# Kernel tuning notes

Measured on AMD Instinct MI355X. Metric: run time of the kernel, lower is better.

The kernel has to match this reference:

```python
import jax, jax.numpy as jnp
import numpy as np

MIN_NORM = 1e-15
EPS = 4e-3  # fp32 boundary epsilon used by HGCN PoincareBall


def _norm(x):
    return jnp.maximum(jnp.linalg.norm(x, axis=-1, keepdims=True), MIN_NORM)


def _artanh(x):
    return jnp.arctanh(jnp.clip(x, -1.0 + 1e-7, 1.0 - 1e-7))


def proj(x, c):
    # clip points to the open Poincare ball of curvature c
    norm = _norm(x)
    maxnorm = (1.0 - EPS) / jnp.sqrt(c)
    return jnp.where(norm > maxnorm, x / norm * maxnorm, x)


def expmap0(u, c):
    sc = jnp.sqrt(c)
    un = _norm(u)
    return jnp.tanh(sc * un) * u / (sc * un)


def logmap0(p, c):
    sc = jnp.sqrt(c)
    pn = _norm(p)
    return _artanh(sc * pn) * p / (pn * sc)


def mobius_add(x, y, c):
    x2 = jnp.sum(x * x, axis=-1, keepdims=True)
    y2 = jnp.sum(y * y, axis=-1, keepdims=True)
    xy = jnp.sum(x * y, axis=-1, keepdims=True)
    num = (1.0 + 2.0 * c * xy + c * y2) * x + (1.0 - c * x2) * y
    den = 1.0 + 2.0 * c * xy + (c ** 2) * x2 * y2
    return num / jnp.maximum(den, MIN_NORM)


def _mobius_from_mx(mx, x, c):
    # shared tail of mobius_matvec: mx is the Euclidean product, x the input points
    sc = jnp.sqrt(c)
    x_norm = _norm(x)            # [..., 1]
    mx_norm = _norm(mx)          # [..., 1]
    res = jnp.tanh(mx_norm / x_norm * _artanh(sc * x_norm)) * mx / (mx_norm * sc)
    zero_row = jnp.all(mx == 0, axis=-1, keepdims=True)
    return jnp.where(zero_row, jnp.zeros_like(res), res)


def mobius_matvec(m, x, c):
    # standard form: mx = x @ m^T   (m: [out, in], x: [N, in])
    return _mobius_from_mx(x @ m.T, x, c)


def hyp_linear(x, W, b, c):
    hw = proj(expmap0(W, c), c)             # proj_tan0 is identity on PoincareBall
    res = proj(mobius_matvec(hw, x, c), c)
    hb = proj(expmap0(b[None, :], c), c)
    return proj(mobius_add(res, hb, c), c)


def hyp_agg(h, adj, W, b, c):
    hw = proj(expmap0(W, c), c)
    support = mobius_matvec(hw, h, c)       # [N, O]
    # mobius_matvec(support, adj, c): Euclidean part is adj @ support,
    # hyperbolic rescale uses row norms of adj (the 'x' argument)
    out = _mobius_from_mx(adj @ support, adj, c)
    out = mobius_add(out, b[None, :], c)    # raw Euclidean bias, as in source
    return proj(out, c)


def hyp_act(h, c):
    xt = jax.nn.leaky_relu(logmap0(h, c))   # default slope 0.01 == F.leaky_relu
    return proj(expmap0(xt, c), 1.0 - c)    # NOTE: source projects with 1-c


def setup_inputs() -> dict:
    key = jax.random.key(0)
    kx, ka, kw1, kw2, kb2 = jax.random.split(key, 5)
    N, IN, OUT = 8192, 512, 128
    x = jax.random.normal(kx, (N, IN), dtype=jnp.float32) * 0.1
    adj = jax.random.uniform(ka, (N, N), dtype=jnp.float32) * (1.0 / N)
    c = jnp.full((1,), 0.7, dtype=jnp.float32)
    glorot = np.sqrt(6.0 / (IN + OUT))
    lin_weight = jax.random.uniform(kw1, (OUT, IN), minval=-glorot, maxval=glorot, dtype=jnp.float32)
    lin_bias = jnp.zeros((OUT,), dtype=jnp.float32)
    stdv = 1.0 / np.sqrt(OUT)
    agg_weight = jax.random.uniform(kw2, (OUT, OUT), minval=-stdv, maxval=stdv, dtype=jnp.float32)
    agg_bias = jax.random.uniform(kb2, (OUT,), minval=-stdv, maxval=stdv, dtype=jnp.float32)
    return {"x": x, "adj": adj, "c": c, "lin_weight": lin_weight, "lin_bias": lin_bias,
            "agg_weight": agg_weight, "agg_bias": agg_bias}


def reference(x, adj, c, lin_weight, lin_bias, agg_weight, agg_bias):
    h = hyp_linear(x, lin_weight, lin_bias, c)
    h = hyp_agg(h, adj, agg_weight, agg_bias, c)
    return hyp_act(h, c)
```

## Files before the change

### kernel.cpp

```cpp
#include <hip/hip_runtime.h>
#include <math.h>


#define MINN 1e-15f

typedef __bf16 bf16x8 __attribute__((ext_vector_type(8)));
typedef float  f32x4  __attribute__((ext_vector_type(4)));

__device__ __forceinline__ unsigned short f2bf(float f) {
  unsigned int u = __float_as_uint(f);
  u += 0x7FFFu + ((u >> 16) & 1u);
  return (unsigned short)(u >> 16);
}

__device__ __forceinline__ unsigned pk_trunc(float lo, float hi) {
  return __builtin_amdgcn_perm(__float_as_uint(hi), __float_as_uint(lo),
                               0x07060302u);
}

__device__ __forceinline__ float artanh_clip(float z) {
  const float B = (float)(1.0 - 1e-7);
  z = fminf(fmaxf(z, -B), B);
  return 0.5f * logf((1.0f + z) / (1.0f - z));
}

__device__ __forceinline__ float red16(float v) {
  v += __shfl_xor(v, 1, 16);
  v += __shfl_xor(v, 2, 16);
  v += __shfl_xor(v, 4, 16);
  v += __shfl_xor(v, 8, 16);
  return v;
}
__device__ __forceinline__ int red16_and(int v) {
  v &= __shfl_xor(v, 1, 16);
  v &= __shfl_xor(v, 2, 16);
  v &= __shfl_xor(v, 4, 16);
  v &= __shfl_xor(v, 8, 16);
  return v;
}
__device__ __forceinline__ float red8(float v) {
  v += __shfl_xor(v, 1, 8);
  v += __shfl_xor(v, 2, 8);
  v += __shfl_xor(v, 4, 8);
  return v;
}
__device__ __forceinline__ int red8_and(int v) {
  v &= __shfl_xor(v, 1, 8);
  v &= __shfl_xor(v, 2, 8);
  v &= __shfl_xor(v, 4, 8);
  return v;
}

__device__ __forceinline__ float block_reduce_128(float v, float* red, int t) {
  #pragma unroll
  for (int m = 1; m < 64; m <<= 1) v += __shfl_xor(v, m, 64);
  if ((t & 63) == 0) red[t >> 6] = v;
  __syncthreads();
  return red[0] + red[1];
}

__device__ __forceinline__ size_t bswz(int k, int n) {
  return ((size_t)(((k >> 5) * 8 + (n >> 4)) * 64 + ((k >> 3) & 3) * 16 +
                   (n & 15))) * 8 + (k & 7);
}

__global__ __launch_bounds__(128) void prep_kernel(
    const float* __restrict__ lw, const float* __restrict__ aw,
    const float* __restrict__ lb, const float* __restrict__ cp,
    unsigned short* __restrict__ B1, unsigned short* __restrict__ B2,
    float* __restrict__ hb)
{
  const float c  = cp[0];
  const float sc = sqrtf(c);
  const float maxn = 0.996f / sc;
  const int b = blockIdx.x, t = threadIdx.x;
  __shared__ float red[2];

  if (b < 128) {
    const int o = b;
    float4 v = ((const float4*)(lw + (size_t)o * 512))[t];
    float ss = block_reduce_128(v.x*v.x + v.y*v.y + v.z*v.z + v.w*v.w, red, t);
    float un = fmaxf(sqrtf(ss), MINN);
    float f  = tanhf(sc * un) / (sc * un);
    float nn = f * un;
    if (nn > maxn) f *= maxn / nn;
    float vals[4] = {v.x, v.y, v.z, v.w};
    #pragma unroll
    for (int i = 0; i < 4; ++i)
      B1[bswz(4 * t + i, o)] = f2bf(f * vals[i]);
  } else if (b < 256) {
    const int n = b - 128;
    float v = aw[(size_t)n * 128 + t];
    float ss = block_reduce_128(v * v, red, t);
    float un = fmaxf(sqrtf(ss), MINN);
    float f  = tanhf(sc * un) / (sc * un);
    float nn = f * un;
    if (nn > maxn) f *= maxn / nn;
    B2[bswz(t, n)] = f2bf(f * v);
  } else {
    float v = lb[t];
    float ss = block_reduce_128(v * v, red, t);
    float un = fmaxf(sqrtf(ss), MINN);
    float f  = tanhf(sc * un) / (sc * un);
    float nn = f * un;
    if (nn > maxn) f *= maxn / nn;
    hb[t] = f * v;
  }
}

__global__ __launch_bounds__(256, 2) void hyp_fused12(
    const float* __restrict__ x, const bf16x8* __restrict__ B1f,
    const bf16x8* __restrict__ B2f, const float* __restrict__ cp,
    const float* __restrict__ hbv, unsigned short* __restrict__ B3)
{
  __shared__ __align__(16) float part[4][16][132];
  __shared__ float asw[4][16];
  __shared__ __align__(16) unsigned short h_lds[16][136];
  const int t = threadIdx.x;
  const int w = t >> 6, lane = t & 63;
  const int quad = lane >> 4, l15 = lane & 15;
  const int row0 = blockIdx.x * 16;
  const float c = cp[0], sc = sqrtf(c), maxn = 0.996f / sc;

  f32x4 acc[8] = {};
  float as4[4] = {};
  const float*  Ap = x + (size_t)(row0 + l15) * 512 + w * 128 + quad * 8;
  const bf16x8* Bp = B1f + (size_t)(w * 4) * 512 + lane;

  #pragma unroll
  for (int s = 0; s < 4; ++s) {
    float4 x0 = *(const float4*)(Ap + s * 32);
    float4 x1 = *(const float4*)(Ap + s * 32 + 4);
    as4[0] = fmaf(x0.x, x0.x, fmaf(x0.y, x0.y, as4[0]));
    as4[1] = fmaf(x0.z, x0.z, fmaf(x0.w, x0.w, as4[1]));
    as4[2] = fmaf(x1.x, x1.x, fmaf(x1.y, x1.y, as4[2]));
    as4[3] = fmaf(x1.z, x1.z, fmaf(x1.w, x1.w, as4[3]));
    union { unsigned short us[8]; bf16x8 v; } pk;
    pk.us[0] = f2bf(x0.x); pk.us[1] = f2bf(x0.y);
    pk.us[2] = f2bf(x0.z); pk.us[3] = f2bf(x0.w);
    pk.us[4] = f2bf(x1.x); pk.us[5] = f2bf(x1.y);
    pk.us[6] = f2bf(x1.z); pk.us[7] = f2bf(x1.w);
    #pragma unroll
    for (int i = 0; i < 8; ++i)
      acc[i] = __builtin_amdgcn_mfma_f32_16x16x32_bf16(
                   pk.v, Bp[(size_t)s * 512 + i * 64], acc[i], 0, 0, 0);
  }
  float asum = (as4[0] + as4[1]) + (as4[2] + as4[3]);
  asum += __shfl_xor(asum, 16, 64);
  asum += __shfl_xor(asum, 32, 64);
  #pragma unroll
  for (int i = 0; i < 8; ++i)
    #pragma unroll
    for (int r = 0; r < 4; ++r)
      part[w][quad * 4 + r][i * 16 + l15] = acc[i][r];
  if (lane < 16) asw[w][l15] = asum;
  __syncthreads();

  const int row = t >> 4, j0 = t & 15;
  float v[8];
  #pragma unroll
  for (int i = 0; i < 8; ++i)
    v[i] = part[0][row][j0 * 8 + i] + part[1][row][j0 * 8 + i]
         + part[2][row][j0 * 8 + i] + part[3][row][j0 * 8 + i];
  const float xss = asw[0][row] + asw[1][row] + asw[2][row] + asw[3][row];

  float mxss_l = 0.f; int zf = 1;
  #pragma unroll
  for (int i = 0; i < 8; ++i) { mxss_l += v[i] * v[i]; zf &= (v[i] == 0.f); }
  const float mxss = red16(mxss_l);
  zf = red16_and(zf);

  const float xn  = fmaxf(sqrtf(xss), MINN);
  const float mxn = fmaxf(sqrtf(mxss), MINN);
  float f1 = 0.f;
  if (!zf) f1 = tanhf(mxn / xn * artanh_clip(sc * xn)) / (mxn * sc);

  float g = f1;
  {
    float rn = f1 * mxn;
    if (rn > maxn) g = f1 * (maxn / rn);
  }
  float yv[8];
  {
    float4 q0 = ((const float4*)hbv)[j0 * 2];
    float4 q1 = ((const float4*)hbv)[j0 * 2 + 1];
    yv[0]=q0.x; yv[1]=q0.y; yv[2]=q0.z; yv[3]=q0.w;
    yv[4]=q1.x; yv[5]=q1.y; yv[6]=q1.z; yv[7]=q1.w;
  }
  float xy_l = 0.f, y2_l = 0.f, o8[8];
  #pragma unroll
  for (int i = 0; i < 8; ++i) {
    o8[i] = g * v[i];
    xy_l += o8[i] * yv[i];
    y2_l += yv[i] * yv[i];
  }
  const float xy = red16(xy_l), y2 = red16(y2_l);
  const float x2 = g * g * mxss;
  const float den = fmaxf(1.0f + 2.0f * c * xy + c * c * x2 * y2, MINN);
  const float ca = (1.0f + 2.0f * c * xy + c * y2) / den;
  const float cb = (1.0f - c * x2) / den;
  float h8[8]; float hss_l = 0.f;
  #pragma unroll
  for (int i = 0; i < 8; ++i) {
    h8[i] = ca * o8[i] + cb * yv[i];
    hss_l += h8[i] * h8[i];
  }
  const float hss = red16(hss_l);
  const float hn  = fmaxf(sqrtf(hss), MINN);
  const float s2  = (hn > maxn) ? maxn / hn : 1.0f;
  const float hn2 = fmaxf(s2 * hn, MINN);

  {
    union { unsigned short us[8]; uint4 q; } hp;
    #pragma unroll
    for (int i = 0; i < 8; ++i) hp.us[i] = f2bf(s2 * h8[i]);
    *(uint4*)&h_lds[row][j0 * 8] = hp.q;
  }
  __syncthreads();

  const bf16x8 av2 = *(const bf16x8*)&h_lds[l15][w * 32 + quad * 8];
  f32x4 acc2[8] = {};
  #pragma unroll
  for (int i = 0; i < 8; ++i)
    acc2[i] = __builtin_amdgcn_mfma_f32_16x16x32_bf16(
                  av2, B2f[(size_t)(w * 8 + i) * 64 + lane], acc2[i], 0, 0, 0);
  #pragma unroll
  for (int i = 0; i < 8; ++i)
    #pragma unroll
    for (int r = 0; r < 4; ++r)
      part[w][quad * 4 + r][i * 16 + l15] = acc2[i][r];
  __syncthreads();

  float v2[8];
  #pragma unroll
  for (int i = 0; i < 8; ++i)
    v2[i] = part[0][row][j0 * 8 + i] + part[1][row][j0 * 8 + i]
          + part[2][row][j0 * 8 + i] + part[3][row][j0 * 8 + i];
  float m2l = 0.f; int zf2 = 1;
  #pragma unroll
  for (int i = 0; i < 8; ++i) { m2l += v2[i] * v2[i]; zf2 &= (v2[i] == 0.f); }
  const float mx2ss = red16(m2l);
  zf2 = red16_and(zf2);
  const float mx2n = fmaxf(sqrtf(mx2ss), MINN);
  float f2 = 0.f;
  if (!zf2) f2 = tanhf(mx2n / hn2 * artanh_clip(sc * hn2)) / (mx2n * sc);

  const int k = row0 + row;
  const size_t base = ((size_t)(((k >> 5) * 8 + (j0 >> 1)) * 64 +
                       ((k >> 3) & 3) * 16 + 8 * (j0 & 1))) * 8 + (k & 7);
  #pragma unroll
  for (int i = 0; i < 8; ++i)
    B3[base + (size_t)i * 8] = f2bf(f2 * v2[i]);
}

#define G3_COMPUTE(U)                                                        \
  {                                                                          \
    float4 x0 = a0[U], x1 = a1[U];                                           \
    as4[0] = fmaf(x0.x, x0.x, fmaf(x0.y, x0.y, as4[0]));                     \
    as4[1] = fmaf(x0.z, x0.z, fmaf(x0.w, x0.w, as4[1]));                     \
    as4[2] = fmaf(x1.x, x1.x, fmaf(x1.y, x1.y, as4[2]));                     \
    as4[3] = fmaf(x1.z, x1.z, fmaf(x1.w, x1.w, as4[3]));                     \
    union { unsigned u32[4]; bf16x8 v; } pk;                                 \
    pk.u32[0] = pk_trunc(x0.x, x0.y);                                        \
    pk.u32[1] = pk_trunc(x0.z, x0.w);                                        \
    pk.u32[2] = pk_trunc(x1.x, x1.y);                                        \
    pk.u32[3] = pk_trunc(x1.z, x1.w);                                        \
    _Pragma("unroll")                                                        \
    for (int i = 0; i < 8; ++i)                                              \
      acc[i] = __builtin_amdgcn_mfma_f32_16x16x32_bf16(pk.v, b[(U) & 3][i],  \
                                                       acc[i], 0, 0, 0);     \
  }

__global__ __launch_bounds__(256, 1) void hyp_gemm3(
    const float* __restrict__ A, const bf16x8* __restrict__ Bf,
    const float* __restrict__ cp, const float* __restrict__ yvec,
    float* __restrict__ out)
{
  __shared__ __align__(16) float part[4][16][132];
  __shared__ float asw[4][16];
  const int t = threadIdx.x;
  const int w = t >> 6, lane = t & 63;
  const int quad = lane >> 4, l15 = lane & 15;
  const int rh = w >> 1, kh = w & 1;
  const int rowbase = blockIdx.x * 32;
  const int row0 = rowbase + rh * 16;
  const float c = cp[0], sc = sqrtf(c), maxn = 0.996f / sc;

  const int k0w = kh * 4096;
  f32x4 acc[8] = {};
  float as4[4] = {};
  const float*  Ap = A + (size_t)(row0 + l15) * 8192 + k0w + quad * 8;
  const bf16x8* Bp = Bf + (size_t)(k0w >> 5) * 512 + lane;

  float4 a0[8], a1[8];
  bf16x8 b[4][8];
  #pragma unroll
  for (int p = 0; p < 8; ++p) {
    a0[p] = *(const float4*)(Ap + p * 32);
    a1[p] = *(const float4*)(Ap + p * 32 + 4);
  }
  #pragma unroll
  for (int p = 0; p < 4; ++p)
    #pragma unroll
    for (int i = 0; i < 8; ++i) b[p][i] = Bp[(size_t)p * 512 + i * 64];

  for (int s = 0; s < 120; s += 8) {
    #pragma unroll
    for (int u = 0; u < 8; ++u) {
      const int sv = s + u;
      G3_COMPUTE(u);
      a0[u] = *(const float4*)(Ap + (size_t)(sv + 8) * 32);
      a1[u] = *(const float4*)(Ap + (size_t)(sv + 8) * 32 + 4);
      #pragma unroll
      for (int i = 0; i < 8; ++i)
        b[u & 3][i] = Bp[(size_t)(sv + 4) * 512 + i * 64];
    }
  }
  #pragma unroll
  for (int u = 0; u < 8; ++u) {
    G3_COMPUTE(u);
    if (u < 4) {
      #pragma unroll
      for (int i = 0; i < 8; ++i)
        b[u & 3][i] = Bp[(size_t)(124 + u) * 512 + i * 64];
    }
  }

  float asum = (as4[0] + as4[1]) + (as4[2] + as4[3]);
  asum += __shfl_xor(asum, 16, 64);
  asum += __shfl_xor(asum, 32, 64);
  #pragma unroll
  for (int i = 0; i < 8; ++i)
    #pragma unroll
    for (int r = 0; r < 4; ++r)
      part[w][quad * 4 + r][i * 16 + l15] = acc[i][r];
  if (lane < 16) asw[w][l15] = asum;
  __syncthreads();

  const int row = t >> 3, j0 = t & 7;
  const int rh2 = row >> 4, rr = row & 15;
  float v[16];
  #pragma unroll
  for (int i = 0; i < 4; ++i) {
    float4 qa = *(const float4*)&part[rh2 * 2][rr][j0 * 16 + 4 * i];
    float4 qb = *(const float4*)&part[rh2 * 2 + 1][rr][j0 * 16 + 4 * i];
    v[4*i+0] = qa.x + qb.x; v[4*i+1] = qa.y + qb.y;
    v[4*i+2] = qa.z + qb.z; v[4*i+3] = qa.w + qb.w;
  }
  const float xss = asw[rh2 * 2][rr] + asw[rh2 * 2 + 1][rr];

  float mxss_l = 0.f; int zf = 1;
  #pragma unroll
  for (int i = 0; i < 16; ++i) { mxss_l += v[i] * v[i]; zf &= (v[i] == 0.f); }
  const float mxss = red8(mxss_l);
  zf = red8_and(zf);

  const float xn  = fmaxf(sqrtf(xss), MINN);
  const float mxn = fmaxf(sqrtf(mxss), MINN);
  float f1 = 0.f;
  if (!zf) f1 = tanhf(mxn / xn * artanh_clip(sc * xn)) / (mxn * sc);

  float yv[16];
  #pragma unroll
  for (int i = 0; i < 4; ++i) {
    float4 q = ((const float4*)yvec)[j0 * 4 + i];
    yv[4*i+0] = q.x; yv[4*i+1] = q.y; yv[4*i+2] = q.z; yv[4*i+3] = q.w;
  }

  float xy_l = 0.f, y2_l = 0.f, o16[16];
  #pragma unroll
  for (int i = 0; i < 16; ++i) {
    o16[i] = f1 * v[i];
    xy_l += o16[i] * yv[i];
    y2_l += yv[i] * yv[i];
  }
  const float xy = red8(xy_l), y2 = red8(y2_l);
  const float x2 = f1 * f1 * mxss;
  const float den = fmaxf(1.0f + 2.0f * c * xy + c * c * x2 * y2, MINN);
  const float ca = (1.0f + 2.0f * c * xy + c * y2) / den;
  const float cb = (1.0f - c * x2) / den;
  float h16[16]; float hss_l = 0.f;
  #pragma unroll
  for (int i = 0; i < 16; ++i) {
    h16[i] = ca * o16[i] + cb * yv[i];
    hss_l += h16[i] * h16[i];
  }
  const float hss = red8(hss_l);
  const float hn  = fmaxf(sqrtf(hss), MINN);
  const float s2  = (hn > maxn) ? maxn / hn : 1.0f;

  const float pn = fmaxf(s2 * hn, MINN);
  const float lf = artanh_clip(sc * pn) / (pn * sc);
  float xt[16]; float uss_l = 0.f;
  #pragma unroll
  for (int i = 0; i < 16; ++i) {
    float l = lf * (s2 * h16[i]);
    xt[i] = (l >= 0.f) ? l : 0.01f * l;
    uss_l += xt[i] * xt[i];
  }
  const float uss = red8(uss_l);
  const float un  = fmaxf(sqrtf(uss), MINN);
  const float ef  = tanhf(sc * un) / (sc * un);
  const float on  = ef * un;
  const float maxn2 = 0.996f / sqrtf(1.0f - c);
  const float s3 = (on > maxn2) ? maxn2 / on : 1.0f;

  float* orow = out + (size_t)(rowbase + row) * 128 + j0 * 16;
  #pragma unroll
  for (int i = 0; i < 4; ++i)
    *(float4*)(orow + 4 * i) = make_float4(
        s3 * ef * xt[4*i+0], s3 * ef * xt[4*i+1],
        s3 * ef * xt[4*i+2], s3 * ef * xt[4*i+3]);
}

extern "C" void kernel_launch(void* const* d_in, const int* in_sizes, int n_in,
                              void* d_out, int out_size, void* d_ws, size_t ws_size,
                              hipStream_t stream)
{
  const float* x   = (const float*)d_in[0];
  const float* adj = (const float*)d_in[1];
  const float* cp  = (const float*)d_in[2];
  const float* lw  = (const float*)d_in[3];
  const float* lb  = (const float*)d_in[4];
  const float* aw  = (const float*)d_in[5];
  const float* ab  = (const float*)d_in[6];
  float* out = (float*)d_out;

  char* ws = (char*)d_ws;
  unsigned short* B1sw = (unsigned short*)(ws);
  unsigned short* B2sw = (unsigned short*)(ws + 131072);
  unsigned short* B3sw = (unsigned short*)(ws + 163840);
  float*          hb   = (float*)(ws + 2260992);

  prep_kernel<<<257, 128, 0, stream>>>(lw, aw, lb, cp, B1sw, B2sw, hb);
  hyp_fused12<<<512, 256, 0, stream>>>(x, (const bf16x8*)B1sw,
                                       (const bf16x8*)B2sw, cp, hb, B3sw);
  hyp_gemm3<<<256, 256, 0, stream>>>(adj, (const bf16x8*)B3sw, cp, ab, out);
}
```

Before: 436.2 us.

## Restructure adjacency GEMM to stage A through double-buffered LDS with 8 waves

The big adj@support kernel moves from 4 waves holding fp32 A tiles and B fragments in registers, with a split-K reduction, to 8 waves. These waves cooperatively load A rows, convert them to bf16 and stage them in a double-buffered LDS tile. Each wave then computes a 16x32 output slice over the full K range, so the split-K partial sums are no longer needed. The goal is to cut register pressure, raise occupancy with launch_bounds(512,2), and give coalesced full-row A streaming. The cost is a barrier per K window, with B fragments now reloaded per wave instead of held in registers.

```diff
diff --git a/kernel.cpp b/kernel.cpp
--- a/kernel.cpp
+++ b/kernel.cpp
@@ -36,18 +36,6 @@
   v &= __shfl_xor(v, 2, 16);
   v &= __shfl_xor(v, 4, 16);
   v &= __shfl_xor(v, 8, 16);
-  return v;
-}
-__device__ __forceinline__ float red8(float v) {
-  v += __shfl_xor(v, 1, 8);
-  v += __shfl_xor(v, 2, 8);
-  v += __shfl_xor(v, 4, 8);
-  return v;
-}
-__device__ __forceinline__ int red8_and(int v) {
-  v &= __shfl_xor(v, 1, 8);
-  v &= __shfl_xor(v, 2, 8);
-  v &= __shfl_xor(v, 4, 8);
   return v;
 }
 
@@ -253,164 +241,162 @@
     B3[base + (size_t)i * 8] = f2bf(f2 * v2[i]);
 }
 
-#define G3_COMPUTE(U)                                                        \
-  {                                                                          \
-    float4 x0 = a0[U], x1 = a1[U];                                           \
-    as4[0] = fmaf(x0.x, x0.x, fmaf(x0.y, x0.y, as4[0]));                     \
-    as4[1] = fmaf(x0.z, x0.z, fmaf(x0.w, x0.w, as4[1]));                     \
-    as4[2] = fmaf(x1.x, x1.x, fmaf(x1.y, x1.y, as4[2]));                     \
-    as4[3] = fmaf(x1.z, x1.z, fmaf(x1.w, x1.w, as4[3]));                     \
-    union { unsigned u32[4]; bf16x8 v; } pk;                                 \
-    pk.u32[0] = pk_trunc(x0.x, x0.y);                                        \
-    pk.u32[1] = pk_trunc(x0.z, x0.w);                                        \
-    pk.u32[2] = pk_trunc(x1.x, x1.y);                                        \
-    pk.u32[3] = pk_trunc(x1.z, x1.w);                                        \
-    _Pragma("unroll")                                                        \
-    for (int i = 0; i < 8; ++i)                                              \
-      acc[i] = __builtin_amdgcn_mfma_f32_16x16x32_bf16(pk.v, b[(U) & 3][i],  \
-                                                       acc[i], 0, 0, 0);     \
-  }
-
-__global__ __launch_bounds__(256, 1) void hyp_gemm3(
+__global__ __launch_bounds__(512, 2) void hyp_gemm3(
     const float* __restrict__ A, const bf16x8* __restrict__ Bf,
     const float* __restrict__ cp, const float* __restrict__ yvec,
     float* __restrict__ out)
 {
-  __shared__ __align__(16) float part[4][16][132];
-  __shared__ float asw[4][16];
+  __shared__ __align__(16) unsigned short a_lds[2][32][264];
   const int t = threadIdx.x;
   const int w = t >> 6, lane = t & 63;
   const int quad = lane >> 4, l15 = lane & 15;
-  const int rh = w >> 1, kh = w & 1;
-  const int rowbase = blockIdx.x * 32;
-  const int row0 = rowbase + rh * 16;
+  const int wm = w >> 2, wn = w & 3;
+  const int row0 = blockIdx.x * 32;
   const float c = cp[0], sc = sqrtf(c), maxn = 0.996f / sc;
 
-  const int k0w = kh * 4096;
-  f32x4 acc[8] = {};
+  f32x4 acc[2] = {};
   float as4[4] = {};
-  const float*  Ap = A + (size_t)(row0 + l15) * 8192 + k0w + quad * 8;
-  const bf16x8* Bp = Bf + (size_t)(k0w >> 5) * 512 + lane;
-
-  float4 a0[8], a1[8];
-  bf16x8 b[4][8];
-  #pragma unroll
-  for (int p = 0; p < 8; ++p) {
-    a0[p] = *(const float4*)(Ap + p * 32);
-    a1[p] = *(const float4*)(Ap + p * 32 + 4);
-  }
-  #pragma unroll
-  for (int p = 0; p < 4; ++p)
-    #pragma unroll
-    for (int i = 0; i < 8; ++i) b[p][i] = Bp[(size_t)p * 512 + i * 64];
-
-  for (int s = 0; s < 120; s += 8) {
-    #pragma unroll
-    for (int u = 0; u < 8; ++u) {
-      const int sv = s + u;
-      G3_COMPUTE(u);
-      a0[u] = *(const float4*)(Ap + (size_t)(sv + 8) * 32);
-      a1[u] = *(const float4*)(Ap + (size_t)(sv + 8) * 32 + 4);
+  const float* Ap = A + (size_t)(row0 + 4 * w) * 8192 + lane * 4;
+  const bf16x8* Bw = Bf + (size_t)(2 * wn) * 64 + lane;
+
+  {
+    float4 aR[4];
+    #pragma unroll
+    for (int j = 0; j < 4; ++j) aR[j] = *(const float4*)(Ap + j * 8192);
+    #pragma unroll
+    for (int j = 0; j < 4; ++j) {
+      as4[j] = fmaf(aR[j].x, aR[j].x, fmaf(aR[j].y, aR[j].y,
+               fmaf(aR[j].z, aR[j].z, fmaf(aR[j].w, aR[j].w, as4[j]))));
+      *(uint2*)&a_lds[0][4 * w + j][lane * 4] =
+          make_uint2(pk_trunc(aR[j].x, aR[j].y), pk_trunc(aR[j].z, aR[j].w));
+    }
+  }
+  __syncthreads();
+
+  for (int win = 0; win < 32; ++win) {
+    const int cur = win & 1;
+    bf16x8 b[8][2];
+    #pragma unroll
+    for (int ks = 0; ks < 8; ++ks) {
+      b[ks][0] = Bw[(size_t)((win * 8 + ks) * 8 + 0) * 64];
+      b[ks][1] = Bw[(size_t)((win * 8 + ks) * 8 + 1) * 64];
+    }
+    float4 aR[4];
+    if (win < 31) {
       #pragma unroll
-      for (int i = 0; i < 8; ++i)
-        b[u & 3][i] = Bp[(size_t)(sv + 4) * 512 + i * 64];
+      for (int j = 0; j < 4; ++j)
+        aR[j] = *(const float4*)(Ap + j * 8192 + (size_t)(win + 1) * 256);
     }
-  }
-  #pragma unroll
-  for (int u = 0; u < 8; ++u) {
-    G3_COMPUTE(u);
-    if (u < 4) {
+    #pragma unroll
+    for (int ks = 0; ks < 8; ++ks) {
+      bf16x8 af = *(const bf16x8*)
+          &a_lds[cur][16 * wm + l15][ks * 32 + quad * 8];
+      acc[0] = __builtin_amdgcn_mfma_f32_16x16x32_bf16(af, b[ks][0], acc[0],
+                                                       0, 0, 0);
+      acc[1] = __builtin_amdgcn_mfma_f32_16x16x32_bf16(af, b[ks][1], acc[1],
+                                                       0, 0, 0);
+    }
+    if (win < 31) {
       #pragma unroll
-      for (int i = 0; i < 8; ++i)
-        b[u & 3][i] = Bp[(size_t)(124 + u) * 512 + i * 64];
+      for (int j = 0; j < 4; ++j) {
+        as4[j] = fmaf(aR[j].x, aR[j].x, fmaf(aR[j].y, aR[j].y,
+                 fmaf(aR[j].z, aR[j].z, fmaf(aR[j].w, aR[j].w, as4[j]))));
+        *(uint2*)&a_lds[cur ^ 1][4 * w + j][lane * 4] =
+            make_uint2(pk_trunc(aR[j].x, aR[j].y), pk_trunc(aR[j].z, aR[j].w));
+      }
     }
-  }
-
-  float asum = (as4[0] + as4[1]) + (as4[2] + as4[3]);
-  asum += __shfl_xor(asum, 16, 64);
-  asum += __shfl_xor(asum, 32, 64);
-  #pragma unroll
-  for (int i = 0; i < 8; ++i)
+    __syncthreads();
+  }
+
+  float (*part)[132] = (float (*)[132]) & a_lds[0][0][0];
+  float* asw = (float*)&a_lds[0][0][0] + 32 * 132;
+
+  #pragma unroll
+  for (int i = 0; i < 2; ++i)
     #pragma unroll
     for (int r = 0; r < 4; ++r)
-      part[w][quad * 4 + r][i * 16 + l15] = acc[i][r];
-  if (lane < 16) asw[w][l15] = asum;
-  __syncthreads();
-
-  const int row = t >> 3, j0 = t & 7;
-  const int rh2 = row >> 4, rr = row & 15;
-  float v[16];
-  #pragma unroll
-  for (int i = 0; i < 4; ++i) {
-    float4 qa = *(const float4*)&part[rh2 * 2][rr][j0 * 16 + 4 * i];
-    float4 qb = *(const float4*)&part[rh2 * 2 + 1][rr][j0 * 16 + 4 * i];
-    v[4*i+0] = qa.x + qb.x; v[4*i+1] = qa.y + qb.y;
-    v[4*i+2] = qa.z + qb.z; v[4*i+3] = qa.w + qb.w;
-  }
-  const float xss = asw[rh2 * 2][rr] + asw[rh2 * 2 + 1][rr];
+      part[16 * wm + quad * 4 + r][32 * wn + 16 * i + l15] = acc[i][r];
+  #pragma unroll
+  for (int j = 0; j < 4; ++j) {
+    float s = as4[j];
+    #pragma unroll
+    for (int m = 1; m < 64; m <<= 1) s += __shfl_xor(s, m, 64);
+    if (lane == 0) asw[4 * w + j] = s;
+  }
+  __syncthreads();
+
+  const int row = t >> 4, j0 = t & 15;
+  float v[8];
+  {
+    float4 q0 = *(const float4*)&part[row][j0 * 8];
+    float4 q1 = *(const float4*)&part[row][j0 * 8 + 4];
+    v[0]=q0.x; v[1]=q0.y; v[2]=q0.z; v[3]=q0.w;
+    v[4]=q1.x; v[5]=q1.y; v[6]=q1.z; v[7]=q1.w;
+  }
+  const float xss = asw[row];
 
   float mxss_l = 0.f; int zf = 1;
   #pragma unroll
-  for (int i = 0; i < 16; ++i) { mxss_l += v[i] * v[i]; zf &= (v[i] == 0.f); }
-  const float mxss = red8(mxss_l);
-  zf = red8_and(zf);
+  for (int i = 0; i < 8; ++i) { mxss_l += v[i] * v[i]; zf &= (v[i] == 0.f); }
+  const float mxss = red16(mxss_l);
+  zf = red16_and(zf);
 
   const float xn  = fmaxf(sqrtf(xss), MINN);
   const float mxn = fmaxf(sqrtf(mxss), MINN);
   float f1 = 0.f;
   if (!zf) f1 = tanhf(mxn / xn * artanh_clip(sc * xn)) / (mxn * sc);
 
-  float yv[16];
-  #pragma unroll
-  for (int i = 0; i < 4; ++i) {
-    float4 q = ((const float4*)yvec)[j0 * 4 + i];
-    yv[4*i+0] = q.x; yv[4*i+1] = q.y; yv[4*i+2] = q.z; yv[4*i+3] = q.w;
-  }
-
-  float xy_l = 0.f, y2_l = 0.f, o16[16];
-  #pragma unroll
-  for (int i = 0; i < 16; ++i) {
-    o16[i] = f1 * v[i];
-    xy_l += o16[i] * yv[i];
+  float yv[8];
+  {
+    float4 q0 = ((const float4*)yvec)[j0 * 2];
+    float4 q1 = ((const float4*)yvec)[j0 * 2 + 1];
+    yv[0]=q0.x; yv[1]=q0.y; yv[2]=q0.z; yv[3]=q0.w;
+    yv[4]=q1.x; yv[5]=q1.y; yv[6]=q1.z; yv[7]=q1.w;
+  }
+
+  float xy_l = 0.f, y2_l = 0.f, o8[8];
+  #pragma unroll
+  for (int i = 0; i < 8; ++i) {
+    o8[i] = f1 * v[i];
+    xy_l += o8[i] * yv[i];
     y2_l += yv[i] * yv[i];
   }
-  const float xy = red8(xy_l), y2 = red8(y2_l);
+  const float xy = red16(xy_l), y2 = red16(y2_l);
   const float x2 = f1 * f1 * mxss;
   const float den = fmaxf(1.0f + 2.0f * c * xy + c * c * x2 * y2, MINN);
   const float ca = (1.0f + 2.0f * c * xy + c * y2) / den;
   const float cb = (1.0f - c * x2) / den;
-  float h16[16]; float hss_l = 0.f;
-  #pragma unroll
-  for (int i = 0; i < 16; ++i) {
-    h16[i] = ca * o16[i] + cb * yv[i];
-    hss_l += h16[i] * h16[i];
-  }
-  const float hss = red8(hss_l);
+  float h8[8]; float hss_l = 0.f;
+  #pragma unroll
+  for (int i = 0; i < 8; ++i) {
+    h8[i] = ca * o8[i] + cb * yv[i];
+    hss_l += h8[i] * h8[i];
+  }
+  const float hss = red16(hss_l);
   const float hn  = fmaxf(sqrtf(hss), MINN);
   const float s2  = (hn > maxn) ? maxn / hn : 1.0f;
 
   const float pn = fmaxf(s2 * hn, MINN);
   const float lf = artanh_clip(sc * pn) / (pn * sc);
-  float xt[16]; float uss_l = 0.f;
-  #pragma unroll
-  for (int i = 0; i < 16; ++i) {
-    float l = lf * (s2 * h16[i]);
+  float xt[8]; float uss_l = 0.f;
+  #pragma unroll
+  for (int i = 0; i < 8; ++i) {
+    float l = lf * (s2 * h8[i]);
     xt[i] = (l >= 0.f) ? l : 0.01f * l;
     uss_l += xt[i] * xt[i];
   }
-  const float uss = red8(uss_l);
+  const float uss = red16(uss_l);
   const float un  = fmaxf(sqrtf(uss), MINN);
   const float ef  = tanhf(sc * un) / (sc * un);
   const float on  = ef * un;
   const float maxn2 = 0.996f / sqrtf(1.0f - c);
   const float s3 = (on > maxn2) ? maxn2 / on : 1.0f;
 
-  float* orow = out + (size_t)(rowbase + row) * 128 + j0 * 16;
-  #pragma unroll
-  for (int i = 0; i < 4; ++i)
-    *(float4*)(orow + 4 * i) = make_float4(
-        s3 * ef * xt[4*i+0], s3 * ef * xt[4*i+1],
-        s3 * ef * xt[4*i+2], s3 * ef * xt[4*i+3]);
+  float* orow = out + (size_t)(row0 + row) * 128 + j0 * 8;
+  *(float4*)orow =
+      make_float4(s3*ef*xt[0], s3*ef*xt[1], s3*ef*xt[2], s3*ef*xt[3]);
+  *(float4*)(orow + 4) =
+      make_float4(s3*ef*xt[4], s3*ef*xt[5], s3*ef*xt[6], s3*ef*xt[7]);
 }
 
 extern "C" void kernel_launch(void* const* d_in, const int* in_sizes, int n_in,
@@ -435,5 +421,5 @@
   prep_kernel<<<257, 128, 0, stream>>>(lw, aw, lb, cp, B1sw, B2sw, hb);
   hyp_fused12<<<512, 256, 0, stream>>>(x, (const bf16x8*)B1sw,
                                        (const bf16x8*)B2sw, cp, hb, B3sw);
-  hyp_gemm3<<<256, 256, 0, stream>>>(adj, (const bf16x8*)B3sw, cp, ab, out);
-}
+  hyp_gemm3<<<256, 512, 0, stream>>>(adj, (const bf16x8*)B3sw, cp, ab, out);
+}
```

New measurement: 408.3 us. -6.4%, faster.
